# Kernel tuning notes

Hardware: AMD Instinct MI355X
Metric: run time of the kernel (lower is better)

The kernel has to match this reference:

```python
import jax, jax.numpy as jnp
import numpy as np

EPS = 1e-5

def _layernorm(x, g, b):
    mu = jnp.mean(x, axis=-1, keepdims=True)
    var = jnp.mean(jnp.square(x - mu), axis=-1, keepdims=True)
    return (x - mu) * jax.lax.rsqrt(var + EPS) * g + b

def setup_inputs() -> dict:
    S, B, D, H, F = 4096, 2, 512, 8, 2048
    key = jax.random.key(0)
    ks = jax.random.split(key, 10)
    sc = 0.02
    return {
        "src": jax.random.normal(ks[0], (S, B, D), jnp.float32),
        "qkv_w": jax.random.normal(ks[1], (3 * D, D), jnp.float32) * sc,
        "qkv_b": jnp.zeros((3 * D,), jnp.float32),
        "out_w": jax.random.normal(ks[2], (D, D), jnp.float32) * sc,
        "w1": jax.random.normal(ks[3], (F, D), jnp.float32) * sc,
        "b1": jnp.zeros((F,), jnp.float32),
        "w2": jax.random.normal(ks[4], (D, F), jnp.float32) * sc,
        "b2": jnp.zeros((D,), jnp.float32),
        "ln1_g": jnp.ones((D,), jnp.float32),
        "ln1_b": jnp.zeros((D,), jnp.float32),
        "ln2_g": jnp.ones((D,), jnp.float32),
        "ln2_b": jnp.zeros((D,), jnp.float32),
    }

def reference(src, qkv_w, qkv_b, out_w, w1, b1, w2, b2, ln1_g, ln1_b, ln2_g, ln2_b):
    S, B, D = src.shape
    H = 8
    hd = D // H
    # --- self attention (NOTE: no 1/sqrt(hd) scaling, matching source) ---
    qkv = src @ qkv_w.T + qkv_b                      # [S, B, 3D]
    q, k, v = jnp.split(qkv, 3, axis=-1)             # each [S, B, D]
    # [S, B*H, hd] -> [B*H, S, hd]
    q = q.reshape(S, B * H, hd).transpose(1, 0, 2)
    k = k.reshape(S, B * H, hd).transpose(1, 0, 2)
    v = v.reshape(S, B * H, hd).transpose(1, 0, 2)
    scores = jnp.einsum('nqd,nkd->nqk', q, k)        # [B*H, S, S]
    attn = jax.nn.softmax(scores, axis=-1)           # dropout = identity (eval)
    out = jnp.einsum('nqk,nkd->nqd', attn, v)        # [B*H, S, hd]
    out = out.transpose(1, 0, 2).reshape(S, B, D)
    attn_out = out @ out_w.T                         # out_proj has no bias
    # --- post-norm residual + FFN ---
    x = _layernorm(src + attn_out, ln1_g, ln1_b)
    ffn = jax.nn.relu(x @ w1.T + b1) @ w2.T + b2
    x = _layernorm(x + ffn, ln2_g, ln2_b)
    return x
```

## Files before the change

kernel.cpp:

```cpp
#include <hip/hip_runtime.h>
#include <cstdint>
#include <math.h>

#define CF4(p) (*reinterpret_cast<const float4*>(p))
#define F4(p)  (*reinterpret_cast<float4*>(p))

typedef __attribute__((ext_vector_type(8))) short bf16x8;
typedef __attribute__((ext_vector_type(4))) float f32x4;

__device__ __forceinline__ unsigned short f2bf(float x) {
  union { float f; unsigned int u; } v; v.f = x;
  unsigned int r = v.u + 0x7FFF + ((v.u >> 16) & 1);
  return (unsigned short)(r >> 16);
}

__device__ __forceinline__ int swz(int row, int col) {
  return row * 64 + (col ^ ((row & 7) << 3));
}

__device__ __forceinline__ void gload_lds16(const void* g, void* lds) {
  __builtin_amdgcn_global_load_lds(
      (const __attribute__((address_space(1))) void*)g,
      (__attribute__((address_space(3))) void*)lds, 16, 0, 0);
}

__global__ __launch_bounds__(256) void cvt_all_kernel(
    const float* __restrict__ src,   unsigned short* __restrict__ src_bf,
    const float* __restrict__ qkvw,  unsigned short* __restrict__ qkvw_bf,
    const float* __restrict__ outw,  unsigned short* __restrict__ outw_bf,
    const float* __restrict__ w1,    unsigned short* __restrict__ w1_bf,
    const float* __restrict__ w2,    unsigned short* __restrict__ w2_bf)
{
  int i = blockIdx.x * 256 + threadIdx.x;
  const float* s; unsigned short* d;
  if      (i < 524288) { s = src;  d = src_bf;                        }
  else if (i < 622592) { s = qkvw; d = qkvw_bf; i -= 524288;          }
  else if (i < 655360) { s = outw; d = outw_bf; i -= 622592;          }
  else if (i < 786432) { s = w1;   d = w1_bf;   i -= 655360;          }
  else if (i < 917504) { s = w2;   d = w2_bf;   i -= 786432;          }
  else return;
  float4 a = CF4(&s[i * 8]), b = CF4(&s[i * 8 + 4]);
  union { bf16x8 v; unsigned short u[8]; } w;
  w.u[0] = f2bf(a.x); w.u[1] = f2bf(a.y); w.u[2] = f2bf(a.z); w.u[3] = f2bf(a.w);
  w.u[4] = f2bf(b.x); w.u[5] = f2bf(b.y); w.u[6] = f2bf(b.z); w.u[7] = f2bf(b.w);
  *reinterpret_cast<bf16x8*>(&d[i * 8]) = w.v;
}

template<int BNT, int BIAS, int RELU, int RES, int OBF>
__global__ __launch_bounds__(256, 2) void bgemm_kernel(
    void* __restrict__ Cv, const unsigned short* __restrict__ A,
    const unsigned short* __restrict__ W, const float* __restrict__ bias,
    const float* __restrict__ R, int M, int N, int K)
{
  constexpr int NJ = BNT / 32;
  __shared__ __align__(16) unsigned short As[2][128 * 64];
  __shared__ __align__(16) unsigned short Ws[2][BNT * 64];

  const int t    = threadIdx.x;
  const int lane = t & 63, wid = t >> 6;
  const int g    = lane >> 4, lr = lane & 15;
  const int wm   = wid >> 1,  wn = wid & 1;
  const int m0   = blockIdx.y * 128, n0 = blockIdx.x * BNT;

  const int sr8 = lane >> 3;
  const int sc  = (lane & 7) ^ sr8;
  const unsigned short* Ag = A + (size_t)(m0 + sr8) * K + sc * 8;
  const unsigned short* Wg = W + (size_t)(n0 + sr8) * K + sc * 8;

  f32x4 acc[4][NJ];
#pragma unroll
  for (int mi = 0; mi < 4; ++mi)
#pragma unroll
    for (int nj = 0; nj < NJ; ++nj)
      acc[mi][nj] = (f32x4){0.f, 0.f, 0.f, 0.f};

#define STAGE_G(buf, k0)                                                   \
  {                                                                        \
    _Pragma("unroll")                                                      \
    for (int i = 0; i < 4; ++i) {                                          \
      const int rb = wid * 32 + i * 8;                                     \
      gload_lds16(Ag + (size_t)rb * K + (k0), (void*)&As[buf][rb * 64]);   \
    }                                                                      \
    _Pragma("unroll")                                                      \
    for (int i = 0; i < BNT / 32; ++i) {                                   \
      const int rb = wid * (BNT / 4) + i * 8;                              \
      gload_lds16(Wg + (size_t)rb * K + (k0), (void*)&Ws[buf][rb * 64]);   \
    }                                                                      \
  }

  STAGE_G(0, 0);
  __syncthreads();

  const int nk = K >> 6;
  for (int kt = 0; kt < nk; ++kt) {
    const int cur = kt & 1;
    if (kt + 1 < nk) STAGE_G(cur ^ 1, (kt + 1) * 64);
#pragma unroll
    for (int ks = 0; ks < 2; ++ks) {
      bf16x8 af[4], bfr[NJ];
#pragma unroll
      for (int mi = 0; mi < 4; ++mi) {
        const int row = wm * 64 + mi * 16 + lr;
        af[mi] = *reinterpret_cast<const bf16x8*>(
            &As[cur][row * 64 + (((ks * 4 + g) ^ (row & 7)) * 8)]);
      }
#pragma unroll
      for (int nj = 0; nj < NJ; ++nj) {
        const int row = wn * (BNT / 2) + nj * 16 + lr;
        bfr[nj] = *reinterpret_cast<const bf16x8*>(
            &Ws[cur][row * 64 + (((ks * 4 + g) ^ (row & 7)) * 8)]);
      }
#pragma unroll
      for (int mi = 0; mi < 4; ++mi)
#pragma unroll
        for (int nj = 0; nj < NJ; ++nj)
          acc[mi][nj] = __builtin_amdgcn_mfma_f32_16x16x32_bf16(
              af[mi], bfr[nj], acc[mi][nj], 0, 0, 0);
    }
    __syncthreads();
  }
#undef STAGE_G

#pragma unroll
  for (int mi = 0; mi < 4; ++mi) {
#pragma unroll
    for (int reg = 0; reg < 4; ++reg) {
      const int r = m0 + wm * 64 + mi * 16 + g * 4 + reg;
#pragma unroll
      for (int nj = 0; nj < NJ; ++nj) {
        const int cc = n0 + wn * (BNT / 2) + nj * 16 + lr;
        float v = acc[mi][nj][reg];
        if (BIAS) v += bias[cc];
        if (RES)  v += R[(size_t)r * N + cc];
        if (RELU) v = fmaxf(v, 0.f);
        if (OBF)  ((unsigned short*)Cv)[(size_t)r * N + cc] = f2bf(v);
        else      ((float*)Cv)[(size_t)r * N + cc] = v;
      }
    }
  }
}

__global__ __launch_bounds__(512, 2) void attn_kernel(
    unsigned short* __restrict__ O, const unsigned short* __restrict__ qkv)
{
  const int Bb = 2, LD = 1536, DM = 512;
  const int qt = blockIdx.x;
  const int nh = blockIdx.y;
  const int b = nh >> 3, h = nh & 7;
  const int cq = h * 64, ck = 512 + h * 64, cv = 1024 + h * 64;

  __shared__ __align__(16) unsigned short Ks [2][64 * 64];
  __shared__ __align__(16) unsigned short Vts[2][64 * 64];
  __shared__ __align__(16) unsigned short Ps [256 * 64];

  const int t    = threadIdx.x;
  const int lane = t & 63;
  const int wid  = t >> 6;
  const int g    = lane >> 4;
  const int lr   = lane & 15;
  const int wq0  = wid * 32;

  bf16x8 qf[2][2];
#pragma unroll
  for (int mi = 0; mi < 2; ++mi)
#pragma unroll
    for (int kq = 0; kq < 2; ++kq)
      qf[mi][kq] = *reinterpret_cast<const bf16x8*>(
          &qkv[((size_t)(qt * 256 + wq0 + mi * 16 + lr) * Bb + b) * LD
               + cq + kq * 32 + g * 8]);

  f32x4 o_acc[2][4];
  float lsum[2] = {0.f, 0.f};
#pragma unroll
  for (int mi = 0; mi < 2; ++mi)
#pragma unroll
    for (int dj = 0; dj < 4; ++dj)
      o_acc[mi][dj] = (f32x4){0.f, 0.f, 0.f, 0.f};

  const int sr8 = lane >> 3;
  const int scK = (lane & 7) ^ sr8;
  const int vD0 = wid * 8;
  const int vSr = lane;

#define STAGE_K(buf, kt)                                               \
  {                                                                    \
    const int rb = wid * 8;                                            \
    gload_lds16(&qkv[((size_t)((kt) * 64 + rb + sr8) * Bb + b) * LD    \
                     + ck + scK * 8],                                  \
                (void*)&Ks[buf][rb * 64]);                             \
  }
#define LOAD_V(kt)                                                     \
  {                                                                    \
    vr = *reinterpret_cast<const bf16x8*>(                             \
        &qkv[((size_t)((kt) * 64 + vSr) * Bb + b) * LD + cv + vD0]);   \
  }
#define WRITE_V(buf)                                                   \
  {                                                                    \
    union { bf16x8 v; unsigned short u[8]; } w;                        \
    w.v = vr;                                                          \
    _Pragma("unroll")                                                  \
    for (int j = 0; j < 8; ++j)                                        \
      Vts[buf][swz(vD0 + j, vSr)] = w.u[j];                            \
  }

  bf16x8 vr;
  STAGE_K(0, 0);
  LOAD_V(0);
  WRITE_V(0);
  __syncthreads();

  for (int kt = 0; kt < 64; ++kt) {
    const int cur = kt & 1;
    const bool hasNext = (kt < 63);
    if (hasNext) { STAGE_K(cur ^ 1, kt + 1); LOAD_V(kt + 1); }

    f32x4 sfT[2][4];
#pragma unroll
    for (int mi = 0; mi < 2; ++mi)
#pragma unroll
      for (int nj = 0; nj < 4; ++nj)
        sfT[mi][nj] = (f32x4){0.f, 0.f, 0.f, 0.f};
    __builtin_amdgcn_s_setprio(1);
#pragma unroll
    for (int nj = 0; nj < 4; ++nj) {
#pragma unroll
      for (int kq = 0; kq < 2; ++kq) {
        bf16x8 ak = *reinterpret_cast<const bf16x8*>(
            &Ks[cur][swz(nj * 16 + lr, kq * 32 + g * 8)]);
        sfT[0][nj] = __builtin_amdgcn_mfma_f32_16x16x32_bf16(
            ak, qf[0][kq], sfT[0][nj], 0, 0, 0);
        sfT[1][nj] = __builtin_amdgcn_mfma_f32_16x16x32_bf16(
            ak, qf[1][kq], sfT[1][nj], 0, 0, 0);
      }
    }
    __builtin_amdgcn_s_setprio(0);

#pragma unroll
    for (int mi = 0; mi < 2; ++mi) {
      const int qrow = wq0 + mi * 16 + lr;
#pragma unroll
      for (int nj = 0; nj < 4; ++nj) {
        const float p0 = __expf(sfT[mi][nj][0]);
        const float p1 = __expf(sfT[mi][nj][1]);
        const float p2 = __expf(sfT[mi][nj][2]);
        const float p3 = __expf(sfT[mi][nj][3]);
        lsum[mi] += (p0 + p1) + (p2 + p3);
        unsigned int w0, w1;
        asm("v_cvt_pk_bf16_f32 %0, %1, %2" : "=v"(w0) : "v"(p0), "v"(p1));
        asm("v_cvt_pk_bf16_f32 %0, %1, %2" : "=v"(w1) : "v"(p2), "v"(p3));
        *reinterpret_cast<uint2*>(&Ps[swz(qrow, nj * 16 + g * 4)]) =
            make_uint2(w0, w1);
      }
    }

    __builtin_amdgcn_s_setprio(1);
#pragma unroll
    for (int kks = 0; kks < 2; ++kks) {
      bf16x8 pa0 = *reinterpret_cast<const bf16x8*>(
          &Ps[swz(wq0 +  0 + lr, kks * 32 + g * 8)]);
      bf16x8 pa1 = *reinterpret_cast<const bf16x8*>(
          &Ps[swz(wq0 + 16 + lr, kks * 32 + g * 8)]);
#pragma unroll
      for (int dj = 0; dj < 4; ++dj) {
        bf16x8 vb = *reinterpret_cast<const bf16x8*>(
            &Vts[cur][swz(dj * 16 + lr, kks * 32 + g * 8)]);
        o_acc[0][dj] = __builtin_amdgcn_mfma_f32_16x16x32_bf16(
            pa0, vb, o_acc[0][dj], 0, 0, 0);
        o_acc[1][dj] = __builtin_amdgcn_mfma_f32_16x16x32_bf16(
            pa1, vb, o_acc[1][dj], 0, 0, 0);
      }
    }
    __builtin_amdgcn_s_setprio(0);

    if (hasNext) WRITE_V(cur ^ 1);
    __syncthreads();
  }
#undef STAGE_K
#undef LOAD_V
#undef WRITE_V

#pragma unroll
  for (int mi = 0; mi < 2; ++mi) {
    float rs = lsum[mi];
    rs += __shfl_xor(rs, 16);
    rs += __shfl_xor(rs, 32);
#pragma unroll
    for (int reg = 0; reg < 4; ++reg) {
      const float rsq = __shfl(rs, (lane & 48) + g * 4 + reg);
      const float inv = 1.f / rsq;
      const int q = qt * 256 + wq0 + mi * 16 + g * 4 + reg;
#pragma unroll
      for (int dj = 0; dj < 4; ++dj)
        O[((size_t)q * Bb + b) * DM + h * 64 + dj * 16 + lr] =
            f2bf(o_acc[mi][dj][reg] * inv);
    }
  }
}

template<int WBF>
__global__ __launch_bounds__(256) void ln_kernel(
    float* __restrict__ out, unsigned short* __restrict__ obf,
    const float* __restrict__ in, const float* __restrict__ g,
    const float* __restrict__ bb)
{
  const int w = threadIdx.x >> 6, lane = threadIdx.x & 63;
  const size_t row = (size_t)blockIdx.x * 4 + w;
  const float* xr = in + row * 512;
  float4 v0 = CF4(&xr[lane * 4]);
  float4 v1 = CF4(&xr[256 + lane * 4]);
  float s = v0.x + v0.y + v0.z + v0.w + v1.x + v1.y + v1.z + v1.w;
  float q = v0.x*v0.x + v0.y*v0.y + v0.z*v0.z + v0.w*v0.w
          + v1.x*v1.x + v1.y*v1.y + v1.z*v1.z + v1.w*v1.w;
#pragma unroll
  for (int off = 1; off < 64; off <<= 1) {
    s += __shfl_xor(s, off);
    q += __shfl_xor(q, off);
  }
  const float mu  = s * (1.f / 512.f);
  const float var = q * (1.f / 512.f) - mu * mu;
  const float rst = rsqrtf(var + 1e-5f);
  float4 g0 = CF4(&g[lane * 4]),  g1 = CF4(&g[256 + lane * 4]);
  float4 b0 = CF4(&bb[lane * 4]), b1 = CF4(&bb[256 + lane * 4]);
  float* orow = out + row * 512;
  float4 o0, o1;
  o0.x = (v0.x - mu) * rst * g0.x + b0.x;
  o0.y = (v0.y - mu) * rst * g0.y + b0.y;
  o0.z = (v0.z - mu) * rst * g0.z + b0.z;
  o0.w = (v0.w - mu) * rst * g0.w + b0.w;
  o1.x = (v1.x - mu) * rst * g1.x + b1.x;
  o1.y = (v1.y - mu) * rst * g1.y + b1.y;
  o1.z = (v1.z - mu) * rst * g1.z + b1.z;
  o1.w = (v1.w - mu) * rst * g1.w + b1.w;
  F4(&orow[lane * 4]) = o0;
  F4(&orow[256 + lane * 4]) = o1;
  if (WBF) {
    unsigned short* brow = obf + row * 512;
    ushort4 u0 = make_ushort4(f2bf(o0.x), f2bf(o0.y), f2bf(o0.z), f2bf(o0.w));
    ushort4 u1 = make_ushort4(f2bf(o1.x), f2bf(o1.y), f2bf(o1.z), f2bf(o1.w));
    *reinterpret_cast<ushort4*>(&brow[lane * 4]) = u0;
    *reinterpret_cast<ushort4*>(&brow[256 + lane * 4]) = u1;
  }
}

extern "C" void kernel_launch(void* const* d_in, const int* in_sizes, int n_in,
                              void* d_out, int out_size, void* d_ws, size_t ws_size,
                              hipStream_t stream)
{
  const float* src   = (const float*)d_in[0];
  const float* qkv_w = (const float*)d_in[1];
  const float* qkv_b = (const float*)d_in[2];
  const float* out_w = (const float*)d_in[3];
  const float* w1    = (const float*)d_in[4];
  const float* b1    = (const float*)d_in[5];
  const float* w2    = (const float*)d_in[6];
  const float* b2    = (const float*)d_in[7];
  const float* ln1g  = (const float*)d_in[8];
  const float* ln1b  = (const float*)d_in[9];
  const float* ln2g  = (const float*)d_in[10];
  const float* ln2b  = (const float*)d_in[11];
  float* out = (float*)d_out;

  const int M = 8192;

  char* ws = (char*)d_ws;
  unsigned short* qkv_bf  = (unsigned short*)(ws + 0);
  unsigned short* attn_bf = (unsigned short*)(ws + 25165824);
  unsigned short* h_bf    = (unsigned short*)(ws + 0);
  float*          y       = (float*)(ws + 33554432);
  float*          z       = (float*)(ws + 33554432);
  float*          x       = (float*)(ws + 50331648);
  unsigned short* x_bf    = (unsigned short*)(ws + 67108864);
  unsigned short* src_bf  = (unsigned short*)(ws + 75497472);
  unsigned short* wqkv_bf = (unsigned short*)(ws + 83886080);
  unsigned short* wout_bf = (unsigned short*)(ws + 85458944);
  unsigned short* w1_bf   = (unsigned short*)(ws + 85983232);
  unsigned short* w2_bf   = (unsigned short*)(ws + 88080384);
  if (ws_size < (size_t)90177536) return;

  dim3 blk(256);

  cvt_all_kernel<<<dim3(3584), blk, 0, stream>>>(
      src, src_bf, qkv_w, wqkv_bf, out_w, wout_bf, w1, w1_bf, w2, w2_bf);

  bgemm_kernel<128,1,0,0,1><<<dim3(12, 64), blk, 0, stream>>>(
      qkv_bf, src_bf, wqkv_bf, qkv_b, nullptr, M, 1536, 512);
  attn_kernel<<<dim3(16, 16), dim3(512), 0, stream>>>(attn_bf, qkv_bf);
  bgemm_kernel<64,0,0,1,0><<<dim3(8, 64), blk, 0, stream>>>(
      y, attn_bf, wout_bf, nullptr, src, M, 512, 512);
  ln_kernel<1><<<dim3(M / 4), blk, 0, stream>>>(x, x_bf, y, ln1g, ln1b);
  bgemm_kernel<128,1,1,0,1><<<dim3(16, 64), blk, 0, stream>>>(
      h_bf, x_bf, w1_bf, b1, nullptr, M, 2048, 512);
  bgemm_kernel<64,1,0,1,0><<<dim3(8, 64), blk, 0, stream>>>(
      z, h_bf, w2_bf, b2, x, M, 512, 2048);
  ln_kernel<0><<<dim3(M / 4), blk, 0, stream>>>(out, nullptr, z, ln2g, ln2b);
}
```

Baseline: 330.1 us.

## Vectorize GEMM epilogue via transposed MFMA and halve attention query tile

The GEMM swaps the MFMA operands so each lane holds four consecutive output columns. The epilogue can then use float4 bias and residual loads, float4 stores, or packed bf16 stores through v_cvt_pk_bf16_f32, in place of scalar accesses. The attention kernel moves from 512-thread blocks over 256 queries to 256-thread blocks over 128 queries, doubling the grid to 512 blocks; each wave now stages twice as many K and V rows. The aim is cheaper epilogue memory traffic and better CU fill, at the cost of reloading K/V once per query tile, so total K/V reads double.

```diff
diff --git a/kernel.cpp b/kernel.cpp
--- a/kernel.cpp
+++ b/kernel.cpp
@@ -115,7 +115,7 @@
 #pragma unroll
         for (int nj = 0; nj < NJ; ++nj)
           acc[mi][nj] = __builtin_amdgcn_mfma_f32_16x16x32_bf16(
-              af[mi], bfr[nj], acc[mi][nj], 0, 0, 0);
+              bfr[nj], af[mi], acc[mi][nj], 0, 0, 0);
     }
     __syncthreads();
   }
@@ -123,24 +123,38 @@
 
 #pragma unroll
   for (int mi = 0; mi < 4; ++mi) {
-#pragma unroll
-    for (int reg = 0; reg < 4; ++reg) {
-      const int r = m0 + wm * 64 + mi * 16 + g * 4 + reg;
-#pragma unroll
-      for (int nj = 0; nj < NJ; ++nj) {
-        const int cc = n0 + wn * (BNT / 2) + nj * 16 + lr;
-        float v = acc[mi][nj][reg];
-        if (BIAS) v += bias[cc];
-        if (RES)  v += R[(size_t)r * N + cc];
-        if (RELU) v = fmaxf(v, 0.f);
-        if (OBF)  ((unsigned short*)Cv)[(size_t)r * N + cc] = f2bf(v);
-        else      ((float*)Cv)[(size_t)r * N + cc] = v;
-      }
-    }
-  }
-}
-
-__global__ __launch_bounds__(512, 2) void attn_kernel(
+    const int r = m0 + wm * 64 + mi * 16 + lr;
+#pragma unroll
+    for (int nj = 0; nj < NJ; ++nj) {
+      const int c0 = n0 + wn * (BNT / 2) + nj * 16 + g * 4;
+      float4 v = make_float4(acc[mi][nj][0], acc[mi][nj][1],
+                             acc[mi][nj][2], acc[mi][nj][3]);
+      if (BIAS) {
+        float4 bb = CF4(&bias[c0]);
+        v.x += bb.x; v.y += bb.y; v.z += bb.z; v.w += bb.w;
+      }
+      if (RES) {
+        float4 rr = CF4(&R[(size_t)r * N + c0]);
+        v.x += rr.x; v.y += rr.y; v.z += rr.z; v.w += rr.w;
+      }
+      if (RELU) {
+        v.x = fmaxf(v.x, 0.f); v.y = fmaxf(v.y, 0.f);
+        v.z = fmaxf(v.z, 0.f); v.w = fmaxf(v.w, 0.f);
+      }
+      if (OBF) {
+        unsigned int w0, w1;
+        asm("v_cvt_pk_bf16_f32 %0, %1, %2" : "=v"(w0) : "v"(v.x), "v"(v.y));
+        asm("v_cvt_pk_bf16_f32 %0, %1, %2" : "=v"(w1) : "v"(v.z), "v"(v.w));
+        *reinterpret_cast<uint2*>(
+            &((unsigned short*)Cv)[(size_t)r * N + c0]) = make_uint2(w0, w1);
+      } else {
+        F4(&((float*)Cv)[(size_t)r * N + c0]) = v;
+      }
+    }
+  }
+}
+
+__global__ __launch_bounds__(256, 2) void attn_kernel(
     unsigned short* __restrict__ O, const unsigned short* __restrict__ qkv)
 {
   const int Bb = 2, LD = 1536, DM = 512;
@@ -151,7 +165,7 @@
 
   __shared__ __align__(16) unsigned short Ks [2][64 * 64];
   __shared__ __align__(16) unsigned short Vts[2][64 * 64];
-  __shared__ __align__(16) unsigned short Ps [256 * 64];
+  __shared__ __align__(16) unsigned short Ps [128 * 64];
 
   const int t    = threadIdx.x;
   const int lane = t & 63;
@@ -166,7 +180,7 @@
 #pragma unroll
     for (int kq = 0; kq < 2; ++kq)
       qf[mi][kq] = *reinterpret_cast<const bf16x8*>(
-          &qkv[((size_t)(qt * 256 + wq0 + mi * 16 + lr) * Bb + b) * LD
+          &qkv[((size_t)(qt * 128 + wq0 + mi * 16 + lr) * Bb + b) * LD
                + cq + kq * 32 + g * 8]);
 
   f32x4 o_acc[2][4];
@@ -184,26 +198,36 @@
 
 #define STAGE_K(buf, kt)                                               \
   {                                                                    \
-    const int rb = wid * 8;                                            \
-    gload_lds16(&qkv[((size_t)((kt) * 64 + rb + sr8) * Bb + b) * LD    \
-                     + ck + scK * 8],                                  \
-                (void*)&Ks[buf][rb * 64]);                             \
+    _Pragma("unroll")                                                  \
+    for (int i = 0; i < 2; ++i) {                                      \
+      const int rb = wid * 16 + i * 8;                                 \
+      gload_lds16(&qkv[((size_t)((kt) * 64 + rb + sr8) * Bb + b) * LD  \
+                       + ck + scK * 8],                                \
+                  (void*)&Ks[buf][rb * 64]);                           \
+    }                                                                  \
   }
 #define LOAD_V(kt)                                                     \
   {                                                                    \
-    vr = *reinterpret_cast<const bf16x8*>(                             \
-        &qkv[((size_t)((kt) * 64 + vSr) * Bb + b) * LD + cv + vD0]);   \
+    _Pragma("unroll")                                                  \
+    for (int p = 0; p < 2; ++p)                                        \
+      vr[p] = *reinterpret_cast<const bf16x8*>(                        \
+          &qkv[((size_t)((kt) * 64 + vSr) * Bb + b) * LD + cv          \
+               + vD0 + p * 32]);                                       \
   }
 #define WRITE_V(buf)                                                   \
   {                                                                    \
-    union { bf16x8 v; unsigned short u[8]; } w;                        \
-    w.v = vr;                                                          \
     _Pragma("unroll")                                                  \
-    for (int j = 0; j < 8; ++j)                                        \
-      Vts[buf][swz(vD0 + j, vSr)] = w.u[j];                            \
-  }
-
-  bf16x8 vr;
+    for (int p = 0; p < 2; ++p) {                                      \
+      const int d0 = vD0 + p * 32;                                     \
+      union { bf16x8 v; unsigned short u[8]; } w;                      \
+      w.v = vr[p];                                                     \
+      _Pragma("unroll")                                                \
+      for (int j = 0; j < 8; ++j)                                      \
+        Vts[buf][swz(d0 + j, vSr)] = w.u[j];                           \
+    }                                                                  \
+  }
+
+  bf16x8 vr[2];
   STAGE_K(0, 0);
   LOAD_V(0);
   WRITE_V(0);
@@ -288,7 +312,7 @@
     for (int reg = 0; reg < 4; ++reg) {
       const float rsq = __shfl(rs, (lane & 48) + g * 4 + reg);
       const float inv = 1.f / rsq;
-      const int q = qt * 256 + wq0 + mi * 16 + g * 4 + reg;
+      const int q = qt * 128 + wq0 + mi * 16 + g * 4 + reg;
 #pragma unroll
       for (int dj = 0; dj < 4; ++dj)
         O[((size_t)q * Bb + b) * DM + h * 64 + dj * 16 + lr] =
@@ -384,7 +408,7 @@
 
   bgemm_kernel<128,1,0,0,1><<<dim3(12, 64), blk, 0, stream>>>(
       qkv_bf, src_bf, wqkv_bf, qkv_b, nullptr, M, 1536, 512);
-  attn_kernel<<<dim3(16, 16), dim3(512), 0, stream>>>(attn_bf, qkv_bf);
+  attn_kernel<<<dim3(32, 16), blk, 0, stream>>>(attn_bf, qkv_bf);
   bgemm_kernel<64,0,0,1,0><<<dim3(8, 64), blk, 0, stream>>>(
       y, attn_bf, wout_bf, nullptr, src, M, 512, 512);
   ln_kernel<1><<<dim3(M / 4), blk, 0, stream>>>(x, x_bf, y, ln1g, ln1b);
```

New measurement: 336.5 us. About the same (+1.9%).
